# Kernel optimization log

Measured on AMD Instinct MI355X. Metric: run time of the kernel, lower is better.

Reference implementation:

```python
import jax, jax.numpy as jnp
import numpy as np

ORDER = 2  # diffusion steps per support
NUM_LAYERS = 2


def gconv(z, supports, W, b):
    # z: [B,N,C]; supports: [S,N,N]; concat [z, S1 z, S1^2 z, S2 z, S2^2 z] -> dense proj
    feats = [z]
    for si in range(supports.shape[0]):
        s = supports[si]
        zk = z
        for _ in range(ORDER):
            zk = jnp.einsum('mn,bnc->bmc', s, zk)
            feats.append(zk)
    zcat = jnp.concatenate(feats, axis=-1)  # [B,N,C*(1+S*ORDER)]
    return zcat @ W + b


def dcgru_cell(x, h, supports, Wg, bg, Wc, bc):
    H = h.shape[-1]
    zr = jax.nn.sigmoid(gconv(jnp.concatenate([x, h], axis=-1), supports, Wg, bg))
    z, r = zr[..., :H], zr[..., H:]
    hc = jnp.tanh(gconv(jnp.concatenate([x, r * h], axis=-1), supports, Wc, bc))
    return z * h + (1.0 - z) * hc


def setup_inputs() -> dict:
    key = jax.random.key(0)
    ks = jax.random.split(key, 32)
    B, T, N, D_IN, H = 64, 12, 325, 2, 128
    K = 1 + 2 * ORDER  # 5 diffusion matrices
    inp = {}
    inp['source'] = jax.random.normal(ks[0], (B, T, N, D_IN), jnp.float32)
    inp['targets'] = jax.random.normal(ks[1], (B, T, N, D_IN), jnp.float32)
    u = jax.random.uniform(ks[2], (2, N, N), jnp.float32)
    inp['supports'] = u / jnp.sum(u, axis=-1, keepdims=True)  # row-stochastic random walks
    sc = 0.05
    inp['enc_Wg0'] = sc * jax.random.normal(ks[3], ((D_IN + H) * K, 2 * H), jnp.float32)
    inp['enc_bg0'] = jnp.zeros((2 * H,), jnp.float32)
    inp['enc_Wc0'] = sc * jax.random.normal(ks[4], ((D_IN + H) * K, H), jnp.float32)
    inp['enc_bc0'] = jnp.zeros((H,), jnp.float32)
    inp['enc_Wg1'] = sc * jax.random.normal(ks[5], ((H + H) * K, 2 * H), jnp.float32)
    inp['enc_bg1'] = jnp.zeros((2 * H,), jnp.float32)
    inp['enc_Wc1'] = sc * jax.random.normal(ks[6], ((H + H) * K, H), jnp.float32)
    inp['enc_bc1'] = jnp.zeros((H,), jnp.float32)
    inp['dec_Wg0'] = sc * jax.random.normal(ks[7], ((D_IN + H) * K, 2 * H), jnp.float32)
    inp['dec_bg0'] = jnp.zeros((2 * H,), jnp.float32)
    inp['dec_Wc0'] = sc * jax.random.normal(ks[8], ((D_IN + H) * K, H), jnp.float32)
    inp['dec_bc0'] = jnp.zeros((H,), jnp.float32)
    inp['dec_Wg1'] = sc * jax.random.normal(ks[9], ((H + H) * K, 2 * H), jnp.float32)
    inp['dec_bg1'] = jnp.zeros((2 * H,), jnp.float32)
    inp['dec_Wc1'] = sc * jax.random.normal(ks[10], ((H + H) * K, H), jnp.float32)
    inp['dec_bc1'] = jnp.zeros((H,), jnp.float32)
    inp['Wp'] = sc * jax.random.normal(ks[11], (H, D_IN), jnp.float32)
    inp['bp'] = jnp.zeros((D_IN,), jnp.float32)
    return inp


def _forward(source, targets, supports,
             enc_Wg0, enc_bg0, enc_Wc0, enc_bc0, enc_Wg1, enc_bg1, enc_Wc1, enc_bc1,
             dec_Wg0, dec_bg0, dec_Wc0, dec_bc0, dec_Wg1, dec_bg1, dec_Wc1, dec_bc1,
             Wp, bp):
    B, T_in, N, D_in = source.shape
    T_out = targets.shape[1]
    enc_params = [(enc_Wg0, enc_bg0, enc_Wc0, enc_bc0), (enc_Wg1, enc_bg1, enc_Wc1, enc_bc1)]
    dec_params = [(dec_Wg0, dec_bg0, dec_Wc0, dec_bc0), (dec_Wg1, dec_bg1, dec_Wc1, dec_bc1)]

    # ---- encoder: per layer, scan over time ----
    cur = jnp.swapaxes(source, 0, 1)  # [T,B,N,C]
    enc_finals = []
    for (Wg, bg, Wc, bc) in enc_params:
        H = Wc.shape[-1]
        h0 = jnp.zeros((B, N, H), source.dtype)
        def step(h, xt, Wg=Wg, bg=bg, Wc=Wc, bc=bc):
            h2 = dcgru_cell(xt, h, supports, Wg, bg, Wc, bc)
            return h2, h2
        hT, hs = jax.lax.scan(step, h0, cur)
        enc_finals.append(hT)
        cur = hs

    # ---- decoder (teacher_forcing_ratio = 0 for determinism) ----
    out_dim = Wp.shape[-1]
    go = jnp.zeros((B, N, out_dim), source.dtype)  # GO symbol

    def dec_step(carry, _):
        states, cur_in = carry
        new_states = []
        x = cur_in
        for i, (Wg, bg, Wc, bc) in enumerate(dec_params):
            s = dcgru_cell(x, states[i], supports, Wg, bg, Wc, bc)
            x = s
            new_states.append(s)
        out = jnp.einsum('bnh,ho->bno', x, Wp) + bp  # [B,N,out_dim]
        return (tuple(new_states), out), out

    _, outs = jax.lax.scan(dec_step, (tuple(enc_finals), go), None, length=T_out)
    return jnp.swapaxes(outs, 0, 1)  # [B,T_out,N,out_dim]


def reference(source, targets, supports,
              enc_Wg0, enc_bg0, enc_Wc0, enc_bc0, enc_Wg1, enc_bg1, enc_Wc1, enc_bc1,
              dec_Wg0, dec_bg0, dec_Wc0, dec_bc0, dec_Wg1, dec_bg1, dec_Wc1, dec_bc1,
              Wp, bp):
    return _forward(source, targets, supports,
                    enc_Wg0, enc_bg0, enc_Wc0, enc_bc0, enc_Wg1, enc_bg1, enc_Wc1, enc_bc1,
                    dec_Wg0, dec_bg0, dec_Wc0, dec_bc0, dec_Wg1, dec_bg1, dec_Wc1, dec_bc1,
                    Wp, bp)
```

## Files before the change

### kernel.cpp

```cpp
#include <hip/hip_runtime.h>
#include <hip/hip_bf16.h>

#define B_  64
#define T_  12
#define N_  325
#define DIN 2
#define H_  128
#define BN  (B_*N_)
#define DPITCH 384
#define AROWS 384

typedef __hip_bfloat16 bf16;
typedef unsigned short u16;
typedef __attribute__((ext_vector_type(8))) short short8;
typedef __attribute__((ext_vector_type(4))) float f32x4;

__device__ __forceinline__ float b2f(bf16 v){ return __bfloat162float(v); }
__device__ __forceinline__ u16 f2b(float f){
    __hip_bfloat16 h = __float2bfloat16(f);
    return *reinterpret_cast<u16*>(&h);
}
__device__ __forceinline__ float ldf(const void* p, size_t i, int bf){
    return bf ? b2f(((const bf16*)p)[i]) : ((const float*)p)[i];
}

__device__ __forceinline__ void gl_lds16(const u16* g, u16* l){
    __builtin_amdgcn_global_load_lds(
        (const __attribute__((address_space(1))) unsigned int*)g,
        (__attribute__((address_space(3))) unsigned int*)l, 16, 0, 0);
}

struct FillCfg { u16 *F, *Ft; const float *x, *h; long xbs; int C, KCP, Cpad, Din, b0, nb; };
struct DiffCfg { u16* F; const u16* Ft; int C, KCP, Cpad, coff0, tpb, T, fcmax, nb; };
struct GemmCfg { const u16* Fb; const u16* Wt; const float* bias; float* zr; float* hb;
                 int KCP, rows, gy, ct, nb; };
struct RhCfg  { u16 *F, *Ft; const float *zr, *h; int KCP, Cpad, Din, b0, nb; };

__global__ void sniff(const void* __restrict__ sup, int* __restrict__ flag){
    if (threadIdx.x == 0 && blockIdx.x == 0){
        float sb = 0.f, sf = 0.f;
        for (int n = 0; n < N_; ++n){
            sb += b2f(((const bf16*)sup)[n]);
            sf += ((const float*)sup)[n];
        }
        float db = fabsf(sb - 1.f), df = fabsf(sf - 1.f);
        *flag = (db < df) ? 1 : 0;
    }
}

struct CvtArgs { const void* src[12]; float* dst[12]; int n[12]; };

__global__ void cvt_all(CvtArgs a, const int* __restrict__ flag){
    int ii = blockIdx.y;
    int i  = blockIdx.x*256 + threadIdx.x;
    if (i >= a.n[ii]) return;
    a.dst[ii][i] = ldf(a.src[ii], i, *flag);
}

__global__ void support_prep(const void* __restrict__ sup, const int* __restrict__ flag,
                             float* __restrict__ msq){
    int bf = *flag;
    int s = blockIdx.z;
    int m = blockIdx.y*16 + threadIdx.y;
    int n = blockIdx.x*16 + threadIdx.x;
    __shared__ float As[16][17], Bs[16][17];
    size_t base = (size_t)s*N_*N_;
    float acc = 0.f;
    for (int j0 = 0; j0 < N_; j0 += 16){
        As[threadIdx.y][threadIdx.x] = (m < N_ && j0+threadIdx.x < N_) ? ldf(sup, base + (size_t)m*N_ + j0+threadIdx.x, bf) : 0.f;
        Bs[threadIdx.y][threadIdx.x] = (j0+threadIdx.y < N_ && n < N_) ? ldf(sup, base + (size_t)(j0+threadIdx.y)*N_ + n, bf) : 0.f;
        __syncthreads();
        #pragma unroll
        for (int jj=0; jj<16; ++jj) acc += As[threadIdx.y][jj]*Bs[jj][threadIdx.x];
        __syncthreads();
    }
    if (m < N_ && n < N_){
        msq[(size_t)(2*s  )*N_*N_ + m*N_ + n] = ldf(sup, base + (size_t)m*N_ + n, bf);
        msq[(size_t)(2*s+1)*N_*N_ + m*N_ + n] = acc;
    }
}

__global__ void asq_prep(const float* __restrict__ msq, u16* __restrict__ asq){
    int idx = blockIdx.x*256 + threadIdx.x;
    int total = 4*AROWS*DPITCH;
    if (idx >= total) return;
    int col = idx % DPITCH;
    int rm  = idx / DPITCH;
    int m   = rm % AROWS;
    int k   = rm / AROWS;
    asq[idx] = (m < N_ && col < N_) ? f2b(msq[((size_t)k*N_ + m)*N_ + col]) : 0;
}

__global__ __launch_bounds__(256) void wtrans(const void* __restrict__ W, u16* __restrict__ Wt,
                                              int KC, int Nout, int KCpad,
                                              const int* __restrict__ flag){
    int bf = *flag;
    int k0 = blockIdx.x*64, c0 = blockIdx.y*64;
    int tid = threadIdx.x;
    __shared__ u16 T[64][72];
    #pragma unroll
    for (int it=0; it<2; ++it){
        int lin = it*256 + tid;
        int kl = lin >> 3, seg = lin & 7;
        int gk = k0 + kl, gc = c0 + seg*8;
        u16 tmp[8];
        #pragma unroll
        for (int e=0;e<8;++e) tmp[e] = (gk < KC) ? f2b(ldf(W, (size_t)gk*Nout + gc + e, bf)) : 0;
        *(uint4*)&T[kl][seg*8] = *(const uint4*)tmp;
    }
    __syncthreads();
    #pragma unroll
    for (int it=0; it<2; ++it){
        int lin = it*256 + tid;
        int cl = lin >> 3, seg = lin & 7;
        u16 tmp[8];
        #pragma unroll
        for (int j=0;j<8;++j) tmp[j] = T[seg*8+j][cl];
        *(uint4*)(Wt + (size_t)(c0+cl)*KCpad + k0 + seg*8) = *(const uint4*)tmp;
    }
}

__global__ __launch_bounds__(256) void fill_k(FillCfg ca, FillCfg cb, int na){
    int bi = blockIdx.x;
    FillCfg c = ca;
    if (bi >= na){ c = cb; bi -= na; }
    int gyc  = (c.C + 63) >> 6;
    int nblk = bi % 6;
    int rest = bi / 6;
    int cblk = rest % gyc;
    int bl   = rest / gyc;
    int bg = c.b0 + bl;
    int n0 = nblk*64, c0 = cblk*64;
    int tid = threadIdx.x;
    __shared__ u16 T[64][72];
    #pragma unroll
    for (int it=0; it<2; ++it){
        int lin = it*256 + tid;
        int nl = lin >> 3, seg = lin & 7;
        int gn = n0 + nl;
        u16 tmp[8];
        #pragma unroll
        for (int e=0;e<8;++e){
            int cc = c0 + seg*8 + e;
            float v = 0.f;
            if (gn < N_ && cc < c.C)
                v = (cc < c.Din) ? c.x[(size_t)bg*c.xbs + (size_t)gn*c.Din + cc]
                                 : c.h[((size_t)bg*N_ + gn)*H_ + (cc - c.Din)];
            tmp[e] = f2b(v);
        }
        *(uint4*)&T[nl][seg*8] = *(const uint4*)tmp;
        if (gn < N_){
            int cbase = c0 + seg*8;
            u16* dst = c.F + ((size_t)bl*N_ + gn)*c.KCP + cbase;
            if (cbase + 7 < c.C){
                *(uint4*)dst = *(const uint4*)tmp;
            } else {
                #pragma unroll
                for (int e=0;e<8;++e) if (cbase + e < c.C) dst[e] = tmp[e];
            }
        }
    }
    __syncthreads();
    #pragma unroll
    for (int it=0; it<2; ++it){
        int lin = it*256 + tid;
        int cl = lin >> 3, seg = lin & 7;
        if (c0 + cl < c.C){
            u16 tmp[8];
            #pragma unroll
            for (int j=0;j<8;++j) tmp[j] = T[seg*8+j][cl];
            *(uint4*)(c.Ft + ((size_t)bl*c.Cpad + (size_t)(c0+cl))*DPITCH + n0 + seg*8)
                = *(const uint4*)tmp;
        }
    }
}

__global__ __launch_bounds__(256) void rhfill_k(RhCfg ca, RhCfg cb, int na){
    int bi = blockIdx.x;
    RhCfg c = ca;
    if (bi >= na){ c = cb; bi -= na; }
    int nblk = bi % 6;
    int rest = bi / 6;
    int cblk = rest & 1;
    int bl   = rest >> 1;
    int bg = c.b0 + bl;
    int n0 = nblk*64, ch0 = cblk*64;
    int tid = threadIdx.x;
    __shared__ u16 T[64][72];
    #pragma unroll
    for (int it=0; it<2; ++it){
        int lin = it*256 + tid;
        int nl = lin >> 3, seg = lin & 7;
        int gn = n0 + nl;
        u16 tmp[8];
        if (gn < N_){
            size_t rloc = (size_t)bl*N_ + gn;
            size_t rg   = (size_t)bg*N_ + gn;
            const float* zp = c.zr + rloc*256 + 128 + ch0 + seg*8;
            const float* hp = c.h  + rg*128 + ch0 + seg*8;
            float4 z0 = *(const float4*)zp, z1 = *(const float4*)(zp+4);
            float4 h0 = *(const float4*)hp, h1 = *(const float4*)(hp+4);
            tmp[0]=f2b(z0.x*h0.x); tmp[1]=f2b(z0.y*h0.y);
            tmp[2]=f2b(z0.z*h0.z); tmp[3]=f2b(z0.w*h0.w);
            tmp[4]=f2b(z1.x*h1.x); tmp[5]=f2b(z1.y*h1.y);
            tmp[6]=f2b(z1.z*h1.z); tmp[7]=f2b(z1.w*h1.w);
            u16* fp = c.F + rloc*c.KCP + c.Din + ch0 + seg*8;
            #pragma unroll
            for (int e=0;e<4;++e){
                unsigned w = (unsigned)tmp[2*e] | ((unsigned)tmp[2*e+1] << 16);
                *(unsigned*)(fp + 2*e) = w;
            }
        } else {
            #pragma unroll
            for (int e=0;e<8;++e) tmp[e] = 0;
        }
        *(uint4*)&T[nl][seg*8] = *(const uint4*)tmp;
    }
    __syncthreads();
    #pragma unroll
    for (int it=0; it<2; ++it){
        int lin = it*256 + tid;
        int cl = lin >> 3, seg = lin & 7;
        u16 tmp[8];
        #pragma unroll
        for (int j=0;j<8;++j) tmp[j] = T[seg*8+j][cl];
        size_t row = (size_t)bl*c.Cpad + c.Din + ch0 + cl;
        *(uint4*)(c.Ft + row*DPITCH + n0 + seg*8) = *(const uint4*)tmp;
    }
}

__global__ __launch_bounds__(256) void diffuse_k(DiffCfg ca, DiffCfg cb, int na,
                                                 const u16* __restrict__ asq){
    int bi = blockIdx.x;
    DiffCfg c = ca;
    if (bi >= na){ c = cb; bi -= na; }
    int xcd = bi & 7, m8 = bi >> 3;
    int tg = m8 / 12, s = m8 % 12;
    int t = tg*8 + xcd;
    if (t >= c.T) return;
    int y = s % 3, k = s / 3;
    int fc0;
    if (c.tpb){
        int blb = t / c.tpb, tb = t - blb*c.tpb;
        fc0 = blb*c.Cpad + c.coff0 + tb*64;
    } else {
        fc0 = t*64;
    }
    int bl0  = fc0 / c.Cpad;
    int rem0 = fc0 - bl0*c.Cpad;

    const u16* A    = asq + (size_t)k*AROWS*DPITCH;
    const u16* Bt_g = c.Ft + (size_t)fc0*DPITCH;

    int m0 = y * 128;
    int tid = threadIdx.x;
    int wv = tid >> 6, lane = tid & 63, l15 = lane & 15, quad = lane >> 4;
    int lr = lane >> 3, ls = lane & 7;

    __shared__ u16 As[128*64];
    __shared__ u16 Bs[64*64];

    f32x4 acc[2][4];
    #pragma unroll
    for (int i2=0;i2<2;++i2)
        #pragma unroll
        for (int j=0;j<4;++j) acc[i2][j] = (f32x4){0.f,0.f,0.f,0.f};

    for (int k0 = 0; k0 < N_; k0 += 64){
        #pragma unroll
        for (int j=0;j<4;++j){
            int row = wv*32 + j*8 + lr;
            int seg = ls ^ lr;
            gl_lds16(A + (size_t)(m0+row)*DPITCH + k0 + seg*8, &As[(wv*32 + j*8)*64]);
        }
        #pragma unroll
        for (int j=0;j<2;++j){
            int row = wv*16 + j*8 + lr;
            int seg = ls ^ lr;
            gl_lds16(Bt_g + (size_t)row*DPITCH + k0 + seg*8, &Bs[(wv*16 + j*8)*64]);
        }
        __syncthreads();
        #pragma unroll
        for (int ks = 0; ks < 64; ks += 32){
            int sw = (((ks>>3) + quad) ^ (l15 & 7)) << 3;
            short8 a0 = *(const short8*)&As[(wv*32      + l15)*64 + sw];
            short8 a1 = *(const short8*)&As[(wv*32 + 16 + l15)*64 + sw];
            short8 b0 = *(const short8*)&Bs[(     l15)*64 + sw];
            short8 b1 = *(const short8*)&Bs[(16 + l15)*64 + sw];
            short8 b2 = *(const short8*)&Bs[(32 + l15)*64 + sw];
            short8 b3 = *(const short8*)&Bs[(48 + l15)*64 + sw];
            acc[0][0] = __builtin_amdgcn_mfma_f32_16x16x32_bf16(a0,b0,acc[0][0],0,0,0);
            acc[0][1] = __builtin_amdgcn_mfma_f32_16x16x32_bf16(a0,b1,acc[0][1],0,0,0);
            acc[0][2] = __builtin_amdgcn_mfma_f32_16x16x32_bf16(a0,b2,acc[0][2],0,0,0);
            acc[0][3] = __builtin_amdgcn_mfma_f32_16x16x32_bf16(a0,b3,acc[0][3],0,0,0);
            acc[1][0] = __builtin_amdgcn_mfma_f32_16x16x32_bf16(a1,b0,acc[1][0],0,0,0);
            acc[1][1] = __builtin_amdgcn_mfma_f32_16x16x32_bf16(a1,b1,acc[1][1],0,0,0);
            acc[1][2] = __builtin_amdgcn_mfma_f32_16x16x32_bf16(a1,b2,acc[1][2],0,0,0);
            acc[1][3] = __builtin_amdgcn_mfma_f32_16x16x32_bf16(a1,b3,acc[1][3],0,0,0);
        }
        __syncthreads();
    }
    #pragma unroll
    for (int j=0;j<4;++j){
        int d  = j*16 + l15;
        int cr = rem0 + d;
        int wrap = (cr >= c.Cpad) ? 1 : 0;
        int bl = bl0 + wrap;
        int cc = wrap ? (cr - c.Cpad) : cr;
        int ok = (fc0 + d) < c.fcmax;
        u16* Cm = c.F + (size_t)bl*N_*c.KCP + (size_t)(k+1)*c.C + cc;
        #pragma unroll
        for (int i2=0;i2<2;++i2){
            #pragma unroll
            for (int r=0;r<4;++r){
                int m = m0 + wv*32 + i2*16 + quad*4 + r;
                if (ok && m < N_) Cm[(size_t)m*c.KCP] = f2b(acc[i2][j][r]);
            }
        }
    }
}

template<int MODE>
__global__ __launch_bounds__(256) void gemm_k(GemmCfg ca, GemmCfg cb, int na){
    int bi = blockIdx.x;
    GemmCfg c = ca;
    if (bi >= na){ c = cb; bi -= na; }
    int xcd = bi & 7, q = bi >> 3;
    int cbk = q % c.ct;
    int rt  = (q / c.ct)*8 + xcd;
    if (rt >= c.gy) return;
    int r0 = rt * 64;
    int c0 = cbk * 64;
    int tid = threadIdx.x;
    int wv = tid >> 6, lane = tid & 63, l15 = lane & 15, quad = lane >> 4;
    int lr = lane >> 3, ls = lane & 7;

    __shared__ u16 As[64*64];
    __shared__ u16 Bs[64*64];

    f32x4 acc[4];
    #pragma unroll
    for (int j=0;j<4;++j) acc[j] = (f32x4){0.f,0.f,0.f,0.f};

    for (int k0 = 0; k0 < c.KCP; k0 += 64){
        #pragma unroll
        for (int j=0;j<2;++j){
            int row = wv*16 + j*8 + lr;
            int seg = ls ^ lr;
            gl_lds16(c.Fb + (size_t)(r0+row)*c.KCP + k0 + seg*8, &As[(wv*16 + j*8)*64]);
            gl_lds16(c.Wt + (size_t)(c0+row)*c.KCP + k0 + seg*8, &Bs[(wv*16 + j*8)*64]);
        }
        __syncthreads();
        #pragma unroll
        for (int ks = 0; ks < 64; ks += 32){
            int sw = (((ks>>3) + quad) ^ (l15 & 7)) << 3;
            short8 a0 = *(const short8*)&As[(wv*16 + l15)*64 + sw];
            short8 b0 = *(const short8*)&Bs[(     l15)*64 + sw];
            short8 b1 = *(const short8*)&Bs[(16 + l15)*64 + sw];
            short8 b2 = *(const short8*)&Bs[(32 + l15)*64 + sw];
            short8 b3 = *(const short8*)&Bs[(48 + l15)*64 + sw];
            acc[0] = __builtin_amdgcn_mfma_f32_16x16x32_bf16(a0,b0,acc[0],0,0,0);
            acc[1] = __builtin_amdgcn_mfma_f32_16x16x32_bf16(a0,b1,acc[1],0,0,0);
            acc[2] = __builtin_amdgcn_mfma_f32_16x16x32_bf16(a0,b2,acc[2],0,0,0);
            acc[3] = __builtin_amdgcn_mfma_f32_16x16x32_bf16(a0,b3,acc[3],0,0,0);
        }
        __syncthreads();
    }
    #pragma unroll
    for (int j=0;j<4;++j){
        int cc = c0 + j*16 + l15;
        #pragma unroll
        for (int r=0;r<4;++r){
            int gr = r0 + wv*16 + quad*4 + r;
            if (gr >= c.rows) continue;
            float v = acc[j][r] + c.bias[cc];
            if (MODE == 0){
                v = 1.f/(1.f + __expf(-v));
                c.zr[(size_t)gr*256 + cc] = v;
            } else {
                float hc   = tanhf(v);
                float z    = c.zr[(size_t)gr*256 + cc];
                float hold = c.hb[(size_t)gr*128 + cc];
                c.hb[(size_t)gr*128 + cc] = z*hold + (1.f - z)*hc;
            }
        }
    }
}

__global__ __launch_bounds__(256) void proj(const float* __restrict__ h1,
                                            const float* __restrict__ Wp,
                                            const float* __restrict__ bp,
                                            float* __restrict__ xdec,
                                            float* __restrict__ out, int t){
    int row  = blockIdx.x * 4 + (threadIdx.x >> 6);
    int lane = threadIdx.x & 63;
    float v0 = h1[(size_t)row*128 + lane];
    float v1 = h1[(size_t)row*128 + 64 + lane];
    float w00 = Wp[lane*2+0],      w01 = Wp[lane*2+1];
    float w10 = Wp[(64+lane)*2+0], w11 = Wp[(64+lane)*2+1];
    float a0 = v0*w00 + v1*w10;
    float a1 = v0*w01 + v1*w11;
    #pragma unroll
    for (int off=32; off>0; off>>=1){
        a0 += __shfl_down(a0, off);
        a1 += __shfl_down(a1, off);
    }
    if (lane == 0){
        a0 += bp[0];
        a1 += bp[1];
        xdec[(size_t)row*2+0] = a0;
        xdec[(size_t)row*2+1] = a1;
        int b = row / N_, n = row % N_;
        size_t o = ((size_t)(b*T_ + t)*N_ + n)*2;
        out[o]   = a0;
        out[o+1] = a1;
    }
}

struct Layer {
    u16 *F, *Ft; float *zr; float *h;
    const u16 *Wg, *Wc; const float *bg, *bc;
    int C, KCP, Din, Cpad;
};

extern "C" void kernel_launch(void* const* d_in, const int* in_sizes, int n_in,
                              void* d_out, int out_size, void* d_ws, size_t ws_size,
                              hipStream_t stream){
    float* out = (float*)d_out;

    char* pb = (char*)d_ws;
    auto alloc = [&](size_t bytes)->void*{
        void* r = (void*)pb;
        pb += (bytes + 255) & ~(size_t)255;
        return r;
    };

    int* flag = (int*)alloc(16);
    sniff<<<1, 64, 0, stream>>>(d_in[2], flag);

    const int idxs[11] = {0,4,6,8,10,12,14,16,18,19,20};
    float* cw[21] = {nullptr};
    CvtArgs ca;
    int maxn = 0;
    for (int ii = 0; ii < 11; ++ii){
        int i = idxs[ii];
        int n = in_sizes[i];
        cw[i] = (float*)alloc((size_t)n*4);
        ca.src[ii] = d_in[i];
        ca.dst[ii] = cw[i];
        ca.n[ii]   = n;
        if (n > maxn) maxn = n;
    }
    cvt_all<<<dim3((maxn+255)/256, 11), 256, 0, stream>>>(ca, flag);
    const float* src = cw[0];

    float* msq  = (float*)alloc((size_t)4*N_*N_*4);
    float* h0   = (float*)alloc((size_t)BN*H_*4);
    float* h1   = (float*)alloc((size_t)BN*H_*4);
    float* xdec = (float*)alloc((size_t)BN*DIN*4);
    u16*   asq  = (u16*)alloc((size_t)4*AROWS*DPITCH*2);

    const int widx[8]  = {3,5,7,9,11,13,15,17};
    const int wKC[8]   = {650,650,1280,1280,650,650,1280,1280};
    const int wNout[8] = {256,128,256,128,256,128,256,128};
    u16* wt[8];
    for (int i=0;i<8;++i){
        int KCpad = (wKC[i] + 63) & ~63;
        wt[i] = (u16*)alloc((size_t)wNout[i]*KCpad*2);
        wtrans<<<dim3(KCpad/64, wNout[i]/64), 256, 0, stream>>>(d_in[widx[i]], wt[i], wKC[i], wNout[i], KCpad, flag);
    }

    {
        dim3 g((N_+15)/16, (N_+15)/16, 2), b(16,16);
        support_prep<<<g, b, 0, stream>>>(d_in[2], flag, msq);
        int tot = 4*AROWS*DPITCH;
        asq_prep<<<dim3((tot+255)/256), 256, 0, stream>>>(msq, asq);
    }
    hipMemsetAsync(h0, 0, sizeof(float)*(size_t)BN*H_*2, stream);

    size_t fixed = (size_t)(pb - (char*)d_ws);
    size_t need0 = (size_t)BN*256*4 + (size_t)BN*704*2  + (size_t)B_*130*DPITCH*2;
    size_t need1 = (size_t)BN*256*4 + (size_t)BN*1280*2 + (size_t)B_*256*DPITCH*2;
    bool dual = (fixed + need0 + need1 + (4<<20)) <= ws_size;

    auto mkFill = [&](Layer& L, const float* x, long xbs, int b0, int Bc)->FillCfg{
        return FillCfg{L.F, L.Ft, x, L.h, xbs, L.C, L.KCP, L.Cpad, L.Din, b0,
                       6*((L.C+63)>>6)*Bc};
    };
    auto mkD1 = [&](Layer& L, int Bc)->DiffCfg{
        int fcmax = Bc*L.Cpad;
        int T = fcmax >> 6;
        return DiffCfg{L.F, L.Ft, L.C, L.KCP, L.Cpad, 0, 0, T, fcmax,
                       12*(((T+7)/8)*8)};
    };
    auto mkD2 = [&](Layer& L, int Bc)->DiffCfg{
        int T = Bc*2;
        return DiffCfg{L.F, L.Ft, L.C, L.KCP, L.Cpad, L.Din, 2, T, Bc*L.Cpad,
                       12*(((T+7)/8)*8)};
    };
    auto mkG0 = [&](Layer& L, int b0, int Bc)->GemmCfg{
        int rows = Bc*N_, gy = (rows+63)/64;
        return GemmCfg{L.F, L.Wg, L.bg, L.zr, L.h + (size_t)b0*N_*H_,
                       L.KCP, rows, gy, 4, 8*((gy+7)/8)*4};
    };
    auto mkG1 = [&](Layer& L, int b0, int Bc)->GemmCfg{
        int rows = Bc*N_, gy = (rows+63)/64;
        return GemmCfg{L.F, L.Wc, L.bc, L.zr, L.h + (size_t)b0*N_*H_,
                       L.KCP, rows, gy, 2, 8*((gy+7)/8)*2};
    };
    auto mkRh = [&](Layer& L, int b0, int Bc)->RhCfg{
        return RhCfg{L.F, L.Ft, L.zr, L.h, L.KCP, L.Cpad, L.Din, b0, 12*Bc};
    };
    auto runCellSeq = [&](Layer& L, const float* x, long xbs, int b0, int Bc){
        FillCfg f = mkFill(L, x, xbs, b0, Bc);
        fill_k<<<dim3(f.nb), 256, 0, stream>>>(f, f, f.nb);
        DiffCfg d1 = mkD1(L, Bc);
        diffuse_k<<<dim3(d1.nb), 256, 0, stream>>>(d1, d1, d1.nb, asq);
        GemmCfg g0 = mkG0(L, b0, Bc);
        gemm_k<0><<<dim3(g0.nb), 256, 0, stream>>>(g0, g0, g0.nb);
        RhCfg r = mkRh(L, b0, Bc);
        rhfill_k<<<dim3(r.nb), 256, 0, stream>>>(r, r, r.nb);
        DiffCfg d2 = mkD2(L, Bc);
        diffuse_k<<<dim3(d2.nb), 256, 0, stream>>>(d2, d2, d2.nb, asq);
        GemmCfg g1 = mkG1(L, b0, Bc);
        gemm_k<1><<<dim3(g1.nb), 256, 0, stream>>>(g1, g1, g1.nb);
    };

    if (dual){
        float* zr0 = (float*)alloc((size_t)BN*256*4);
        u16*   F0  = (u16*)alloc((size_t)BN*704*2);
        u16*   Ft0 = (u16*)alloc((size_t)B_*130*DPITCH*2);
        float* zr1 = (float*)alloc((size_t)BN*256*4);
        u16*   F1  = (u16*)alloc((size_t)BN*1280*2);
        u16*   Ft1 = (u16*)alloc((size_t)B_*256*DPITCH*2);
        alloc(1<<19);

        hipMemsetAsync(F0, 0, (size_t)BN*704*2, stream);

        Layer E0{F0, Ft0, zr0, h0, wt[0], wt[1], cw[4],  cw[6],  130, 704,  2,   130};
        Layer E1{F1, Ft1, zr1, h1, wt[2], wt[3], cw[8],  cw[10], 256, 1280, 128, 256};
        Layer D0{F0, Ft0, zr0, h0, wt[4], wt[5], cw[12], cw[14], 130, 704,  2,   130};
        Layer D1{F1, Ft1, zr1, h1, wt[6], wt[7], cw[16], cw[18], 256, 1280, 128, 256};

        for (int s = 0; s <= T_; ++s){
            bool has0 = (s < T_), has1 = (s >= 1);
            const float* x0 = src + (size_t)s*N_*DIN;
            FillCfg f0 = mkFill(E0, x0, (long)T_*N_*DIN, 0, B_);
            FillCfg f1 = mkFill(E1, h0, (long)N_*H_,     0, B_);
            if (has0 && has1) fill_k<<<dim3(f0.nb+f1.nb),256,0,stream>>>(f0, f1, f0.nb);
            else if (has0)    fill_k<<<dim3(f0.nb),256,0,stream>>>(f0, f0, f0.nb);
            else              fill_k<<<dim3(f1.nb),256,0,stream>>>(f1, f1, f1.nb);

            DiffCfg a1 = mkD1(E0, B_), b1 = mkD1(E1, B_);
            if (has0 && has1) diffuse_k<<<dim3(a1.nb+b1.nb),256,0,stream>>>(a1, b1, a1.nb, asq);
            else if (has0)    diffuse_k<<<dim3(a1.nb),256,0,stream>>>(a1, a1, a1.nb, asq);
            else              diffuse_k<<<dim3(b1.nb),256,0,stream>>>(b1, b1, b1.nb, asq);

            GemmCfg ga = mkG0(E0, 0, B_), gb = mkG0(E1, 0, B_);
            if (has0 && has1) gemm_k<0><<<dim3(ga.nb+gb.nb),256,0,stream>>>(ga, gb, ga.nb);
            else if (has0)    gemm_k<0><<<dim3(ga.nb),256,0,stream>>>(ga, ga, ga.nb);
            else              gemm_k<0><<<dim3(gb.nb),256,0,stream>>>(gb, gb, gb.nb);

            RhCfg ra = mkRh(E0, 0, B_), rb = mkRh(E1, 0, B_);
            if (has0 && has1) rhfill_k<<<dim3(ra.nb+rb.nb),256,0,stream>>>(ra, rb, ra.nb);
            else if (has0)    rhfill_k<<<dim3(ra.nb),256,0,stream>>>(ra, ra, ra.nb);
            else              rhfill_k<<<dim3(rb.nb),256,0,stream>>>(rb, rb, rb.nb);

            DiffCfg a2 = mkD2(E0, B_), b2 = mkD2(E1, B_);
            if (has0 && has1) diffuse_k<<<dim3(a2.nb+b2.nb),256,0,stream>>>(a2, b2, a2.nb, asq);
            else if (has0)    diffuse_k<<<dim3(a2.nb),256,0,stream>>>(a2, a2, a2.nb, asq);
            else              diffuse_k<<<dim3(b2.nb),256,0,stream>>>(b2, b2, b2.nb, asq);

            GemmCfg ha = mkG1(E0, 0, B_), hb = mkG1(E1, 0, B_);
            if (has0 && has1) gemm_k<1><<<dim3(ha.nb+hb.nb),256,0,stream>>>(ha, hb, ha.nb);
            else if (has0)    gemm_k<1><<<dim3(ha.nb),256,0,stream>>>(ha, ha, ha.nb);
            else              gemm_k<1><<<dim3(hb.nb),256,0,stream>>>(hb, hb, hb.nb);
        }

        hipMemsetAsync(xdec, 0, sizeof(float)*(size_t)BN*DIN, stream);
        for (int t = 0; t < T_; ++t){
            runCellSeq(D0, xdec, (long)N_*DIN, 0, B_);
            runCellSeq(D1, h0,   (long)N_*H_,  0, B_);
            proj<<<dim3(BN/4), 256, 0, stream>>>(h1, cw[19], cw[20], xdec, out, t);
        }
    } else {
        size_t perb = (size_t)N_*1280*2 + (size_t)N_*256*4 + (size_t)256*DPITCH*2;
        int Bc = 64;
        while (Bc > 2 && fixed + (1<<20) + (size_t)Bc*perb > ws_size) Bc >>= 1;
        float* zr = (float*)alloc((size_t)Bc*N_*256*4);
        u16*   F  = (u16*)alloc((size_t)Bc*N_*1280*2);
        u16*   Ft = (u16*)alloc((size_t)Bc*256*DPITCH*2);
        alloc(1<<19);

        hipMemsetAsync(F, 0, (size_t)Bc*N_*1280*2, stream);

        Layer SE0{F, Ft, zr, h0, wt[0], wt[1], cw[4],  cw[6],  130, 704,  2,   130};
        Layer SE1{F, Ft, zr, h1, wt[2], wt[3], cw[8],  cw[10], 256, 1280, 128, 256};
        Layer SD0{F, Ft, zr, h0, wt[4], wt[5], cw[12], cw[14], 130, 704,  2,   130};
        Layer SD1{F, Ft, zr, h1, wt[6], wt[7], cw[16], cw[18], 256, 1280, 128, 256};

        for (int t = 0; t < T_; ++t){
            for (int b0 = 0; b0 < B_; b0 += Bc)
                runCellSeq(SE0, src + (size_t)t*N_*DIN, (long)T_*N_*DIN, b0, Bc);
            for (int b0 = 0; b0 < B_; b0 += Bc)
                runCellSeq(SE1, h0, (long)N_*H_, b0, Bc);
        }
        hipMemsetAsync(xdec, 0, sizeof(float)*(size_t)BN*DIN, stream);
        for (int t = 0; t < T_; ++t){
            for (int b0 = 0; b0 < B_; b0 += Bc)
                runCellSeq(SD0, xdec, (long)N_*DIN, b0, Bc);
            for (int b0 = 0; b0 < B_; b0 += Bc)
                runCellSeq(SD1, h0, (long)N_*H_, b0, Bc);
            proj<<<dim3(BN/4), 256, 0, stream>>>(h1, cw[19], cw[20], xdec, out, t);
        }
    }
}
```

Before: 5.014 ms.

## Fuse decoder output projection into candidate GEMM epilogue and next fill

In the dual-buffer decoder path, the separate per-step projection kernel is replaced. The layer-1 candidate GEMM epilogue now computes partial projections of the new hidden state for its 64-column tile into a small buffer, and the next step's layer-0 fill kernel sums the partials, adds the bias, writes the output slot and uses the result as the decoder input. This removes 11 kernel launches and a re-read of h1 per step. In exchange the GEMM epilogue gets an extra LDS stage and a serial 64-term dot product on half the threads. The launch-bounds hint is also dropped from rhfill_k.

```diff
diff --git a/kernel.cpp b/kernel.cpp
--- a/kernel.cpp
+++ b/kernel.cpp
@@ -30,10 +30,11 @@
         (__attribute__((address_space(3))) unsigned int*)l, 16, 0, 0);
 }
 
-struct FillCfg { u16 *F, *Ft; const float *x, *h; long xbs; int C, KCP, Cpad, Din, b0, nb; };
+struct FillCfg { u16 *F, *Ft; const float *x, *h; long xbs; int C, KCP, Cpad, Din, b0, nb;
+                 const float *pb, *bpp; float *out; int tslot; };
 struct DiffCfg { u16* F; const u16* Ft; int C, KCP, Cpad, coff0, tpb, T, fcmax, nb; };
 struct GemmCfg { const u16* Fb; const u16* Wt; const float* bias; float* zr; float* hb;
-                 int KCP, rows, gy, ct, nb; };
+                 int KCP, rows, gy, ct, nb; float* pb; const float* Wp; };
 struct RhCfg  { u16 *F, *Ft; const float *zr, *h; int KCP, Cpad, Din, b0, nb; };
 
 __global__ void sniff(const void* __restrict__ sup, int* __restrict__ flag){
@@ -143,9 +144,19 @@
         for (int e=0;e<8;++e){
             int cc = c0 + seg*8 + e;
             float v = 0.f;
-            if (gn < N_ && cc < c.C)
-                v = (cc < c.Din) ? c.x[(size_t)bg*c.xbs + (size_t)gn*c.Din + cc]
-                                 : c.h[((size_t)bg*N_ + gn)*H_ + (cc - c.Din)];
+            if (gn < N_ && cc < c.C){
+                if (cc < c.Din){
+                    if (c.pb){
+                        size_t row = (size_t)bg*N_ + gn;
+                        v = c.pb[row*2 + cc] + c.pb[(size_t)BN*2 + row*2 + cc] + c.bpp[cc];
+                        c.out[((size_t)(bg*T_ + c.tslot)*N_ + gn)*2 + cc] = v;
+                    } else {
+                        v = c.x[(size_t)bg*c.xbs + (size_t)gn*c.Din + cc];
+                    }
+                } else {
+                    v = c.h[((size_t)bg*N_ + gn)*H_ + (cc - c.Din)];
+                }
+            }
             tmp[e] = f2b(v);
         }
         *(uint4*)&T[nl][seg*8] = *(const uint4*)tmp;
@@ -175,7 +186,7 @@
     }
 }
 
-__global__ __launch_bounds__(256) void rhfill_k(RhCfg ca, RhCfg cb, int na){
+__global__ void rhfill_k(RhCfg ca, RhCfg cb, int na){
     int bi = blockIdx.x;
     RhCfg c = ca;
     if (bi >= na){ c = cb; bi -= na; }
@@ -335,8 +346,9 @@
     int wv = tid >> 6, lane = tid & 63, l15 = lane & 15, quad = lane >> 4;
     int lr = lane >> 3, ls = lane & 7;
 
-    __shared__ u16 As[64*64];
-    __shared__ u16 Bs[64*64];
+    __shared__ u16 SM[2*64*64];
+    u16* As = SM;
+    u16* Bs = SM + 64*64;
 
     f32x4 acc[4];
     #pragma unroll
@@ -366,6 +378,7 @@
         }
         __syncthreads();
     }
+    float* ft = (float*)SM;
     #pragma unroll
     for (int j=0;j<4;++j){
         int cc = c0 + j*16 + l15;
@@ -381,7 +394,24 @@
                 float hc   = tanhf(v);
                 float z    = c.zr[(size_t)gr*256 + cc];
                 float hold = c.hb[(size_t)gr*128 + cc];
-                c.hb[(size_t)gr*128 + cc] = z*hold + (1.f - z)*hc;
+                float hnew = z*hold + (1.f - z)*hc;
+                c.hb[(size_t)gr*128 + cc] = hnew;
+                if (MODE == 1 && c.pb)
+                    ft[(wv*16 + quad*4 + r)*64 + (j*16 + l15)] = hnew;
+            }
+        }
+    }
+    if (MODE == 1 && c.pb){
+        __syncthreads();
+        if (tid < 128){
+            int row = tid >> 1, o = tid & 1;
+            int gr = r0 + row;
+            if (gr < c.rows){
+                float s = 0.f;
+                #pragma unroll 8
+                for (int col = 0; col < 64; ++col)
+                    s += ft[row*64 + col] * c.Wp[(size_t)(c0+col)*2 + o];
+                c.pb[(size_t)cbk*BN*2 + (size_t)gr*2 + o] = s;
             }
         }
     }
@@ -458,6 +488,7 @@
     float* h0   = (float*)alloc((size_t)BN*H_*4);
     float* h1   = (float*)alloc((size_t)BN*H_*4);
     float* xdec = (float*)alloc((size_t)BN*DIN*4);
+    float* pbuf = (float*)alloc((size_t)2*BN*2*4);
     u16*   asq  = (u16*)alloc((size_t)4*AROWS*DPITCH*2);
 
     const int widx[8]  = {3,5,7,9,11,13,15,17};
@@ -485,7 +516,7 @@
 
     auto mkFill = [&](Layer& L, const float* x, long xbs, int b0, int Bc)->FillCfg{
         return FillCfg{L.F, L.Ft, x, L.h, xbs, L.C, L.KCP, L.Cpad, L.Din, b0,
-                       6*((L.C+63)>>6)*Bc};
+                       6*((L.C+63)>>6)*Bc, nullptr, nullptr, nullptr, 0};
     };
     auto mkD1 = [&](Layer& L, int Bc)->DiffCfg{
         int fcmax = Bc*L.Cpad;
@@ -501,18 +532,20 @@
     auto mkG0 = [&](Layer& L, int b0, int Bc)->GemmCfg{
         int rows = Bc*N_, gy = (rows+63)/64;
         return GemmCfg{L.F, L.Wg, L.bg, L.zr, L.h + (size_t)b0*N_*H_,
-                       L.KCP, rows, gy, 4, 8*((gy+7)/8)*4};
+                       L.KCP, rows, gy, 4, 8*((gy+7)/8)*4, nullptr, nullptr};
     };
     auto mkG1 = [&](Layer& L, int b0, int Bc)->GemmCfg{
         int rows = Bc*N_, gy = (rows+63)/64;
         return GemmCfg{L.F, L.Wc, L.bc, L.zr, L.h + (size_t)b0*N_*H_,
-                       L.KCP, rows, gy, 2, 8*((gy+7)/8)*2};
+                       L.KCP, rows, gy, 2, 8*((gy+7)/8)*2, nullptr, nullptr};
     };
     auto mkRh = [&](Layer& L, int b0, int Bc)->RhCfg{
         return RhCfg{L.F, L.Ft, L.zr, L.h, L.KCP, L.Cpad, L.Din, b0, 12*Bc};
     };
-    auto runCellSeq = [&](Layer& L, const float* x, long xbs, int b0, int Bc){
+    auto runCellSeq = [&](Layer& L, const float* x, long xbs, int b0, int Bc,
+                          const float* fpb, int tslot, float* g1pb){
         FillCfg f = mkFill(L, x, xbs, b0, Bc);
+        if (fpb){ f.pb = fpb; f.bpp = cw[20]; f.out = out; f.tslot = tslot; }
         fill_k<<<dim3(f.nb), 256, 0, stream>>>(f, f, f.nb);
         DiffCfg d1 = mkD1(L, Bc);
         diffuse_k<<<dim3(d1.nb), 256, 0, stream>>>(d1, d1, d1.nb, asq);
@@ -523,6 +556,7 @@
         DiffCfg d2 = mkD2(L, Bc);
         diffuse_k<<<dim3(d2.nb), 256, 0, stream>>>(d2, d2, d2.nb, asq);
         GemmCfg g1 = mkG1(L, b0, Bc);
+        if (g1pb){ g1.pb = g1pb; g1.Wp = cw[19]; }
         gemm_k<1><<<dim3(g1.nb), 256, 0, stream>>>(g1, g1, g1.nb);
     };
 
@@ -579,10 +613,11 @@
 
         hipMemsetAsync(xdec, 0, sizeof(float)*(size_t)BN*DIN, stream);
         for (int t = 0; t < T_; ++t){
-            runCellSeq(D0, xdec, (long)N_*DIN, 0, B_);
-            runCellSeq(D1, h0,   (long)N_*H_,  0, B_);
-            proj<<<dim3(BN/4), 256, 0, stream>>>(h1, cw[19], cw[20], xdec, out, t);
-        }
+            runCellSeq(D0, xdec, (long)N_*DIN, 0, B_,
+                       (t > 0) ? pbuf : nullptr, t-1, nullptr);
+            runCellSeq(D1, h0, (long)N_*H_, 0, B_, nullptr, 0, pbuf);
+        }
+        proj<<<dim3(BN/4), 256, 0, stream>>>(h1, cw[19], cw[20], xdec, out, T_-1);
     } else {
         size_t perb = (size_t)N_*1280*2 + (size_t)N_*256*4 + (size_t)256*DPITCH*2;
         int Bc = 64;
@@ -601,16 +636,17 @@
 
         for (int t = 0; t < T_; ++t){
             for (int b0 = 0; b0 < B_; b0 += Bc)
-                runCellSeq(SE0, src + (size_t)t*N_*DIN, (long)T_*N_*DIN, b0, Bc);
+                runCellSeq(SE0, src + (size_t)t*N_*DIN, (long)T_*N_*DIN, b0, Bc,
+                           nullptr, 0, nullptr);
             for (int b0 = 0; b0 < B_; b0 += Bc)
-                runCellSeq(SE1, h0, (long)N_*H_, b0, Bc);
+                runCellSeq(SE1, h0, (long)N_*H_, b0, Bc, nullptr, 0, nullptr);
         }
         hipMemsetAsync(xdec, 0, sizeof(float)*(size_t)BN*DIN, stream);
         for (int t = 0; t < T_; ++t){
             for (int b0 = 0; b0 < B_; b0 += Bc)
-                runCellSeq(SD0, xdec, (long)N_*DIN, b0, Bc);
+                runCellSeq(SD0, xdec, (long)N_*DIN, b0, Bc, nullptr, 0, nullptr);
             for (int b0 = 0; b0 < B_; b0 += Bc)
-                runCellSeq(SD1, h0, (long)N_*H_, b0, Bc);
+                runCellSeq(SD1, h0, (long)N_*H_, b0, Bc, nullptr, 0, nullptr);
             proj<<<dim3(BN/4), 256, 0, stream>>>(h1, cw[19], cw[20], xdec, out, t);
         }
     }
```

Result: no change. 5.053 ms (+0.8%).
